# Kernel optimization log

Measured on AMD Instinct MI355X. Metric: run time of the kernel, lower is better.

The kernel has to match this reference:

```python
import jax, jax.numpy as jnp
import numpy as np

B, S, DIN, DQ, DK = 4, 2048, 1024, 64, 64
NEG_INF = -jnp.inf


def _make_mask(sq, sk):
    # Mirrors createMask: causal mask (-inf where key_idx > query_idx),
    # except 3 randomly chosen (row, col) 'global token' pairs left at 0.
    # torch version uses random.sample; we use a fixed numpy RNG for determinism.
    rng = np.random.default_rng(0)
    g_rows = rng.choice(sk, 3, replace=False)  # sampled from range(lrlen)
    g_cols = rng.choice(sq, 3, replace=False)  # sampled from range(sequence_len)
    row = jnp.arange(sq)[:, None]
    col = jnp.arange(sk)[None, :]
    mask = jnp.where(col > row, NEG_INF, 0.0).astype(jnp.float32)
    mask = mask.at[jnp.asarray(g_rows), jnp.asarray(g_cols)].set(0.0)
    return mask  # [sq, sk]


def setup_inputs() -> dict:
    key = jax.random.key(0)
    ks = jax.random.split(key, 9)
    sc = 1.0 / np.sqrt(DIN)
    return {
        "q": jax.random.normal(ks[0], (B, S, DIN), jnp.float32),
        "k": jax.random.normal(ks[1], (B, S, DIN), jnp.float32),
        "v": jax.random.normal(ks[2], (B, S, DIN), jnp.float32),
        "Wq": jax.random.normal(ks[3], (DIN, DQ), jnp.float32) * sc,
        "bq": jax.random.normal(ks[4], (DQ,), jnp.float32) * sc,
        "Wk": jax.random.normal(ks[5], (DIN, DK), jnp.float32) * sc,
        "bk": jax.random.normal(ks[6], (DK,), jnp.float32) * sc,
        "Wv": jax.random.normal(ks[7], (DIN, DK), jnp.float32) * sc,
        "bv": jax.random.normal(ks[8], (DK,), jnp.float32) * sc,
    }


def reference(q, k, v, Wq, bq, Wk, bk, Wv, bv):
    Q = q @ Wq + bq            # [B,S,DQ]
    K = k @ Wk + bk            # [B,S,DK]
    V = v @ Wv + bv            # [B,S,DK]
    scores = jnp.einsum("bqd,bkd->bqk", Q, K)  # [B,S,S]
    mask = _make_mask(scores.shape[-2], scores.shape[-1])
    denom = jnp.asarray(K.shape[-1], jnp.float32) ** 0.5
    # NOTE: original adds mask BEFORE dividing by sqrt(d_k); -inf survives division.
    attn = jax.nn.softmax((scores + mask) / denom, axis=-1)
    return jnp.einsum("bqk,bkd->bqd", attn, V)  # [B,S,DK]
```

## Files before the change

kernel.cpp:

```cpp
#include <hip/hip_runtime.h>
#include <cstdint>
#include <cstddef>
#include <math.h>

#define SEQ    2048
#define NBATCH 4
#define DIN    1024
#define DH     64

typedef __attribute__((ext_vector_type(8))) short  short8;
typedef __attribute__((ext_vector_type(4))) float  floatx4;
typedef __attribute__((ext_vector_type(4))) unsigned short ushort4v;

#define MFMA16(a, b, c) __builtin_amdgcn_mfma_f32_16x16x32_bf16((a), (b), (c), 0, 0, 0)

__device__ __forceinline__ unsigned short f2bf(float x) {
  unsigned u = __float_as_uint(x);
  return (unsigned short)((u + 0x8000u) >> 16);
}
__device__ __forceinline__ float bf2f(unsigned short h) {
  return __uint_as_float(((unsigned)h) << 16);
}

namespace nprng {

struct PCG64 {
  __uint128_t state, inc;
  bool has_uint32;
  uint32_t uinteger;
};

static inline void pcg_step(PCG64 &g) {
  const __uint128_t MULT =
      (((__uint128_t)0x2360ed051fc65da4ULL) << 64) | 0x4385df649fccf645ULL;
  g.state = g.state * MULT + g.inc;
}

static inline uint64_t pcg_output(const PCG64 &g) {
  uint64_t hi = (uint64_t)(g.state >> 64);
  uint64_t lo = (uint64_t)g.state;
  uint64_t x = hi ^ lo;
  unsigned rot = (unsigned)(g.state >> 122) & 63u;
  return (x >> rot) | (x << ((64u - rot) & 63u));
}

static inline uint64_t pcg_next64(PCG64 &g) { pcg_step(g); return pcg_output(g); }

static inline uint32_t pcg_next32(PCG64 &g) {
  if (g.has_uint32) { g.has_uint32 = false; return g.uinteger; }
  uint64_t n = pcg_next64(g);
  g.has_uint32 = true;
  g.uinteger = (uint32_t)(n >> 32);
  return (uint32_t)(n & 0xffffffffu);
}

static inline void pcg_seed_from_seedseq0(PCG64 &g) {
  const uint32_t MULT_A = 0x931e8875u;
  const uint32_t MULT_B = 0x58f38dedu;
  const uint32_t MIX_L  = 0xca01f9ddu;
  const uint32_t MIX_R  = 0x4973f715u;
  uint32_t hc = 0x43b0d7e5u;
  uint32_t pool[4];
  for (int i = 0; i < 4; i++) {
    uint32_t v = 0u;
    v ^= hc; hc *= MULT_A; v *= hc; v ^= v >> 16;
    pool[i] = v;
  }
  for (int is = 0; is < 4; is++) {
    for (int id = 0; id < 4; id++) {
      if (is == id) continue;
      uint32_t h = pool[is];
      h ^= hc; hc *= MULT_A; h *= hc; h ^= h >> 16;
      uint32_t r = (pool[id] * MIX_L) ^ (h * MIX_R);
      r ^= r >> 16;
      pool[id] = r;
    }
  }
  uint32_t hb = 0x8b51f9ddu;
  uint32_t w[8];
  for (int i = 0; i < 8; i++) {
    uint32_t v = pool[i & 3];
    v ^= hb; hb *= MULT_B; v *= hb; v ^= v >> 16;
    w[i] = v;
  }
  uint64_t sv[4];
  for (int k = 0; k < 4; k++)
    sv[k] = (uint64_t)w[2 * k] | ((uint64_t)w[2 * k + 1] << 32);
  __uint128_t initstate = (((__uint128_t)sv[0]) << 64) | sv[1];
  __uint128_t initseq   = (((__uint128_t)sv[2]) << 64) | sv[3];
  g.state = 0; g.inc = (initseq << 1) | 1;
  pcg_step(g);
  g.state += initstate;
  pcg_step(g);
  g.has_uint32 = false; g.uinteger = 0;
}

static inline uint32_t bounded32(PCG64 &g, uint32_t rng ) {
  if (rng == 0) return 0;
  const uint32_t rng_excl = rng + 1u;
  uint64_t m = (uint64_t)pcg_next32(g) * (uint64_t)rng_excl;
  uint32_t leftover = (uint32_t)m;
  if (leftover < rng_excl) {
    const uint32_t threshold = (uint32_t)(0xffffffffu - rng) % rng_excl;
    while (leftover < threshold) {
      m = (uint64_t)pcg_next32(g) * (uint64_t)rng_excl;
      leftover = (uint32_t)m;
    }
  }
  return (uint32_t)(m >> 32);
}

static inline void choice3_2048(PCG64 &g, long long idx[3]) {
  const int pop = 2048, sz = 3;
  uint64_t hs[4] = { (uint64_t)-1, (uint64_t)-1, (uint64_t)-1, (uint64_t)-1 };
  const uint64_t mask = 3;
  for (int j = pop - sz; j < pop; j++) {
    uint64_t val = (uint64_t)bounded32(g, (uint32_t)j);
    uint64_t loc = val & mask;
    while (hs[loc] != (uint64_t)-1 && hs[loc] != val) loc = (loc + 1) & mask;
    if (hs[loc] == (uint64_t)-1) {
      hs[loc] = val;
      idx[j - pop + sz] = (long long)val;
    } else {
      loc = (uint64_t)j & mask;
      while (hs[loc] != (uint64_t)-1) loc = (loc + 1) & mask;
      hs[loc] = (uint64_t)j;
      idx[j - pop + sz] = (long long)j;
    }
  }
  for (int i = 2; i >= 1; i--) {
    uint32_t j = bounded32(g, (uint32_t)i);
    long long t = idx[j]; idx[j] = idx[i]; idx[i] = t;
  }
}

}

__global__ __launch_bounds__(256) void wtrans_kernel(
    const float* __restrict__ Wq, const float* __restrict__ Wk,
    const float* __restrict__ Wv, unsigned short* __restrict__ WT) {
  int idx = blockIdx.x * 256 + threadIdx.x;
  int p   = idx >> 16;
  int rem = idx & 65535;
  int n   = rem >> 10;
  int k   = rem & 1023;
  const float* W = (p == 0) ? Wq : (p == 1) ? Wk : Wv;
  WT[idx] = f2bf(W[k * 64 + n]);
}

__global__ __launch_bounds__(256, 4) void proj_kernel(
    const float* __restrict__ xq, const float* __restrict__ xk,
    const float* __restrict__ xv, const unsigned short* __restrict__ WT,
    const float* __restrict__ bq, const float* __restrict__ bk,
    const float* __restrict__ bv,
    unsigned short* __restrict__ QP, unsigned short* __restrict__ KP,
    unsigned short* __restrict__ VPT) {
  const int proj = blockIdx.y;
  const float* X    = (proj == 0) ? xq : (proj == 1) ? xk : xv;
  const float* bias = (proj == 0) ? bq : (proj == 1) ? bk : bv;

  const int m0   = blockIdx.x * 16;
  const int tid  = threadIdx.x;
  const int w    = tid >> 6;
  const int l    = tid & 63;
  const int quad = l >> 4;
  const int lx   = l & 15;
  const int kb   = w << 8;

  const float* Xr = X + (size_t)(m0 + lx) * DIN + kb + quad * 8;
  const unsigned short* Wb = WT + (size_t)proj * 65536 + kb + quad * 8;
  const unsigned short* Wr0 = Wb + (size_t)(lx)      * 1024;
  const unsigned short* Wr1 = Wb + (size_t)(16 + lx) * 1024;
  const unsigned short* Wr2 = Wb + (size_t)(32 + lx) * 1024;
  const unsigned short* Wr3 = Wb + (size_t)(48 + lx) * 1024;

  floatx4 acc0 = {0.f, 0.f, 0.f, 0.f}, acc1 = acc0, acc2 = acc0, acc3 = acc0;

  float4 xc0 = *(const float4*)(Xr);
  float4 xc1 = *(const float4*)(Xr + 4);
  short8 wc0 = *(const short8*)(Wr0);
  short8 wc1 = *(const short8*)(Wr1);
  short8 wc2 = *(const short8*)(Wr2);
  short8 wc3 = *(const short8*)(Wr3);

  for (int k = 32; k < 256; k += 32) {
    float4 xn0 = *(const float4*)(Xr + k);
    float4 xn1 = *(const float4*)(Xr + k + 4);
    short8 wn0 = *(const short8*)(Wr0 + k);
    short8 wn1 = *(const short8*)(Wr1 + k);
    short8 wn2 = *(const short8*)(Wr2 + k);
    short8 wn3 = *(const short8*)(Wr3 + k);
    short8 af;
    af[0] = f2bf(xc0.x); af[1] = f2bf(xc0.y); af[2] = f2bf(xc0.z); af[3] = f2bf(xc0.w);
    af[4] = f2bf(xc1.x); af[5] = f2bf(xc1.y); af[6] = f2bf(xc1.z); af[7] = f2bf(xc1.w);
    acc0 = MFMA16(af, wc0, acc0);
    acc1 = MFMA16(af, wc1, acc1);
    acc2 = MFMA16(af, wc2, acc2);
    acc3 = MFMA16(af, wc3, acc3);
    xc0 = xn0; xc1 = xn1; wc0 = wn0; wc1 = wn1; wc2 = wn2; wc3 = wn3;
  }
  {
    short8 af;
    af[0] = f2bf(xc0.x); af[1] = f2bf(xc0.y); af[2] = f2bf(xc0.z); af[3] = f2bf(xc0.w);
    af[4] = f2bf(xc1.x); af[5] = f2bf(xc1.y); af[6] = f2bf(xc1.z); af[7] = f2bf(xc1.w);
    acc0 = MFMA16(af, wc0, acc0);
    acc1 = MFMA16(af, wc1, acc1);
    acc2 = MFMA16(af, wc2, acc2);
    acc3 = MFMA16(af, wc3, acc3);
  }

  __shared__ float Cs[4][16][68];
#pragma unroll
  for (int i = 0; i < 4; i++) {
    const int r = quad * 4 + i;
    Cs[w][r][lx]      = acc0[i];
    Cs[w][r][16 + lx] = acc1[i];
    Cs[w][r][32 + lx] = acc2[i];
    Cs[w][r][48 + lx] = acc3[i];
  }
  __syncthreads();

  if (proj < 2) {
    unsigned short* outp = (proj == 0) ? QP : KP;
    const int row = tid >> 4;
    const int d0  = (tid & 15) * 4;
    ushort4v v;
#pragma unroll
    for (int j = 0; j < 4; j++) {
      float s = Cs[0][row][d0 + j] + Cs[1][row][d0 + j] +
                Cs[2][row][d0 + j] + Cs[3][row][d0 + j] + bias[d0 + j];
      v[j] = f2bf(s);
    }
    *(ushort4v*)(outp + (size_t)(m0 + row) * 64 + d0) = v;
  } else {
    const int dim = tid >> 2;
    const int s0  = (tid & 3) * 4;
    const int bq_ = m0 >> 11;
    const int sq  = (m0 & 2047) + s0;
    const float bb = bias[dim];
    ushort4v v;
#pragma unroll
    for (int j = 0; j < 4; j++) {
      float s = Cs[0][s0 + j][dim] + Cs[1][s0 + j][dim] +
                Cs[2][s0 + j][dim] + Cs[3][s0 + j][dim] + bb;
      v[j] = f2bf(s);
    }
    *(ushort4v*)(VPT + ((size_t)bq_ * 64 + dim) * SEQ + sq) = v;
  }
}

__global__ __launch_bounds__(256, 2) void attn_kernel(
    const unsigned short* __restrict__ QP, const unsigned short* __restrict__ KP,
    const unsigned short* __restrict__ VPT, float* __restrict__ out,
    int R0, int C0, int R1, int C1, int R2, int C2) {
  const int b    = blockIdx.y;
  const int bx   = blockIdx.x;
  const int qi   = (bx & 1) ? (127 - (bx >> 1)) : (bx >> 1);
  const int q0   = qi * 16;
  const int tid  = threadIdx.x;
  const int w    = tid >> 6;
  const int l    = tid & 63;
  const int quad = l >> 4;
  const int lx   = l & 15;

  __shared__ unsigned short Ps[4][16][72];
  __shared__ float Os[4][16][64];
  __shared__ float mS[4][16], lS[4][16];
  __shared__ float lgS[3];
  __shared__ int   lgF[3];

  const unsigned short* Qb = QP + ((size_t)b * SEQ + q0) * 64;
  const unsigned short* Kb = KP + (size_t)b * SEQ * 64;
  const unsigned short* Vb = VPT + (size_t)b * 64 * SEQ;

  const short8 aq0 = *(const short8*)(Qb + (size_t)lx * 64 + quad * 8);
  const short8 aq1 = *(const short8*)(Qb + (size_t)lx * 64 + 32 + quad * 8);

  floatx4 O[4];
  float m_i[4], l_i[4];
#pragma unroll
  for (int c = 0; c < 4; c++) O[c] = (floatx4){0.f, 0.f, 0.f, 0.f};
#pragma unroll
  for (int i = 0; i < 4; i++) { m_i[i] = -INFINITY; l_i[i] = 0.f; }

  const int T = (q0 + 79) >> 6;

  for (int t = w; t < T; t += 4) {
    const int k0 = t << 6;
    const bool mT = (t == T - 1);

    short8 kf[8], vf[8];
#pragma unroll
    for (int c = 0; c < 4; c++) {
#pragma unroll
      for (int s = 0; s < 2; s++) {
        kf[c * 2 + s] = *(const short8*)(Kb + (size_t)(k0 + 16 * c + lx) * 64 + s * 32 + quad * 8);
        vf[s * 4 + c] = *(const short8*)(Vb + (size_t)(16 * c + lx) * SEQ + k0 + s * 32 + quad * 8);
      }
    }

    floatx4 sc[4];
#pragma unroll
    for (int c = 0; c < 4; c++) {
      sc[c] = (floatx4){0.f, 0.f, 0.f, 0.f};
      sc[c] = MFMA16(aq0, kf[2 * c], sc[c]);
      sc[c] = MFMA16(aq1, kf[2 * c + 1], sc[c]);
    }

    float mt[4], al[4];
#pragma unroll
    for (int i = 0; i < 4; i++) {
      const int rowg = q0 + quad * 4 + i;
      float vmax = -INFINITY;
#pragma unroll
      for (int c = 0; c < 4; c++) {
        float v = sc[c][i] * 0.125f;
        if (mT && (k0 + 16 * c + lx) > rowg) v = -INFINITY;
        sc[c][i] = v;
        vmax = fmaxf(vmax, v);
      }
      mt[i] = vmax;
    }
#pragma unroll
    for (int i = 0; i < 4; i++) {
#pragma unroll
      for (int off = 8; off >= 1; off >>= 1)
        mt[i] = fmaxf(mt[i], __shfl_xor(mt[i], off));
      const float mn = fmaxf(m_i[i], mt[i]);
      al[i] = __expf(m_i[i] - mn);
      m_i[i] = mn;
      float s = 0.f;
#pragma unroll
      for (int c = 0; c < 4; c++) {
        float p = __expf(sc[c][i] - mn);
        Ps[w][quad * 4 + i][16 * c + lx] = f2bf(p);
        s += p;
      }
#pragma unroll
      for (int off = 8; off >= 1; off >>= 1) s += __shfl_xor(s, off);
      l_i[i] = l_i[i] * al[i] + s;
    }
#pragma unroll
    for (int c = 0; c < 4; c++)
#pragma unroll
      for (int i = 0; i < 4; i++) O[c][i] *= al[i];
    asm volatile("" ::: "memory");
    const short8 pf0 = *(const short8*)&Ps[w][lx][quad * 8];
    const short8 pf1 = *(const short8*)&Ps[w][lx][32 + quad * 8];
#pragma unroll
    for (int c = 0; c < 4; c++) {
      O[c] = MFMA16(pf0, vf[c],     O[c]);
      O[c] = MFMA16(pf1, vf[4 + c], O[c]);
    }
  }

  if (lx == 0) {
#pragma unroll
    for (int i = 0; i < 4; i++) {
      mS[w][quad * 4 + i] = m_i[i];
      lS[w][quad * 4 + i] = l_i[i];
    }
  }
#pragma unroll
  for (int c = 0; c < 4; c++)
#pragma unroll
    for (int i = 0; i < 4; i++) Os[w][quad * 4 + i][16 * c + lx] = O[c][i];

  if (w == 0) {
#pragma unroll
    for (int p = 0; p < 3; p++) {
      const int R = (p == 0) ? R0 : (p == 1) ? R1 : R2;
      const int C = (p == 0) ? C0 : (p == 1) ? C1 : C2;
      const int act = (R >= q0 && R < q0 + 16 && C > R);
      float d = 0.f;
      if (act) {
        const float qv = bf2f(QP[((size_t)b * SEQ + R) * 64 + l]);
        const float kv = bf2f(KP[((size_t)b * SEQ + C) * 64 + l]);
        d = qv * kv;
#pragma unroll
        for (int off = 32; off >= 1; off >>= 1) d += __shfl_xor(d, off);
        d *= 0.125f;
      }
      if (l == 0) { lgF[p] = act; lgS[p] = d; }
    }
  }
  __syncthreads();

  {
    const int row = tid >> 4;
    const int d0  = (tid & 15) * 4;
    const int Rs[3] = {R0, R1, R2};
    const int Cs3[3] = {C0, C1, C2};

    float mf = -INFINITY;
#pragma unroll
    for (int w4 = 0; w4 < 4; w4++) mf = fmaxf(mf, mS[w4][row]);
#pragma unroll
    for (int p = 0; p < 3; p++)
      if (lgF[p] && (Rs[p] - q0) == row) mf = fmaxf(mf, lgS[p]);

    float lf = 0.f;
    float o0 = 0.f, o1 = 0.f, o2 = 0.f, o3 = 0.f;
#pragma unroll
    for (int w4 = 0; w4 < 4; w4++) {
      const float a = __expf(mS[w4][row] - mf);
      lf += a * lS[w4][row];
      const float* op = &Os[w4][row][d0];
      o0 += a * op[0]; o1 += a * op[1]; o2 += a * op[2]; o3 += a * op[3];
    }
#pragma unroll
    for (int p = 0; p < 3; p++) {
      if (lgF[p] && (Rs[p] - q0) == row) {
        const float pe = __expf(lgS[p] - mf);
        lf += pe;
        const int C = Cs3[p];
        o0 += pe * bf2f(Vb[(size_t)(d0 + 0) * SEQ + C]);
        o1 += pe * bf2f(Vb[(size_t)(d0 + 1) * SEQ + C]);
        o2 += pe * bf2f(Vb[(size_t)(d0 + 2) * SEQ + C]);
        o3 += pe * bf2f(Vb[(size_t)(d0 + 3) * SEQ + C]);
      }
    }
    const float inv = 1.0f / lf;
    float4 r;
    r.x = o0 * inv; r.y = o1 * inv; r.z = o2 * inv; r.w = o3 * inv;
    *(float4*)(out + ((size_t)b * SEQ + q0 + row) * 64 + d0) = r;
  }
}

extern "C" void kernel_launch(void* const* d_in, const int* in_sizes, int n_in,
                              void* d_out, int out_size, void* d_ws,
                              size_t ws_size, hipStream_t stream) {
  const float* xq = (const float*)d_in[0];
  const float* xk = (const float*)d_in[1];
  const float* xv = (const float*)d_in[2];
  const float* Wq = (const float*)d_in[3];
  const float* bq = (const float*)d_in[4];
  const float* Wk = (const float*)d_in[5];
  const float* bk = (const float*)d_in[6];
  const float* Wv = (const float*)d_in[7];
  const float* bv = (const float*)d_in[8];
  float* out = (float*)d_out;

  unsigned short* QP  = (unsigned short*)d_ws;
  unsigned short* KP  = QP + (size_t)NBATCH * SEQ * 64;
  unsigned short* VPT = KP + (size_t)NBATCH * SEQ * 64;
  unsigned short* WT  = VPT + (size_t)NBATCH * 64 * SEQ;

  nprng::PCG64 g;
  nprng::pcg_seed_from_seedseq0(g);
  long long rows[3], cols[3];
  nprng::choice3_2048(g, rows);
  nprng::choice3_2048(g, cols);

  wtrans_kernel<<<768, 256, 0, stream>>>(Wq, Wk, Wv, WT);

  dim3 pgrid(512, 3);
  proj_kernel<<<pgrid, 256, 0, stream>>>(xq, xk, xv, WT, bq, bk, bv, QP, KP, VPT);

  dim3 agrid(SEQ / 16, NBATCH);
  attn_kernel<<<agrid, 256, 0, stream>>>(
      QP, KP, VPT, out, (int)rows[0], (int)cols[0], (int)rows[1], (int)cols[1],
      (int)rows[2], (int)cols[2]);
}
```

Before: 188.5 us.

## Restructure projection GEMM to stage X in LDS and split output columns across waves

The projection kernel now processes 32 rows per block instead of 16. X is loaded coalesced, converted to bf16 and staged in shared memory in 256-wide K chunks, with register double-buffering of the next chunk's X and W. Each wave now owns 16 output columns over the full K range instead of a K-slice, so the cross-wave reduction through shared memory goes away. Output stores are widened to 8 elements. The cost is more registers (launch bounds lowered to 3), LDS barriers per chunk, and half as many blocks.

```diff
diff --git a/kernel.cpp b/kernel.cpp
--- a/kernel.cpp
+++ b/kernel.cpp
@@ -148,7 +148,7 @@
   WT[idx] = f2bf(W[k * 64 + n]);
 }
 
-__global__ __launch_bounds__(256, 4) void proj_kernel(
+__global__ __launch_bounds__(256, 3) void proj_kernel(
     const float* __restrict__ xq, const float* __restrict__ xk,
     const float* __restrict__ xv, const unsigned short* __restrict__ WT,
     const float* __restrict__ bq, const float* __restrict__ bk,
@@ -159,93 +159,91 @@
   const float* X    = (proj == 0) ? xq : (proj == 1) ? xk : xv;
   const float* bias = (proj == 0) ? bq : (proj == 1) ? bk : bv;
 
-  const int m0   = blockIdx.x * 16;
+  const int m0   = blockIdx.x * 32;
   const int tid  = threadIdx.x;
   const int w    = tid >> 6;
   const int l    = tid & 63;
   const int quad = l >> 4;
   const int lx   = l & 15;
-  const int kb   = w << 8;
-
-  const float* Xr = X + (size_t)(m0 + lx) * DIN + kb + quad * 8;
-  const unsigned short* Wb = WT + (size_t)proj * 65536 + kb + quad * 8;
-  const unsigned short* Wr0 = Wb + (size_t)(lx)      * 1024;
-  const unsigned short* Wr1 = Wb + (size_t)(16 + lx) * 1024;
-  const unsigned short* Wr2 = Wb + (size_t)(32 + lx) * 1024;
-  const unsigned short* Wr3 = Wb + (size_t)(48 + lx) * 1024;
-
-  floatx4 acc0 = {0.f, 0.f, 0.f, 0.f}, acc1 = acc0, acc2 = acc0, acc3 = acc0;
-
-  float4 xc0 = *(const float4*)(Xr);
-  float4 xc1 = *(const float4*)(Xr + 4);
-  short8 wc0 = *(const short8*)(Wr0);
-  short8 wc1 = *(const short8*)(Wr1);
-  short8 wc2 = *(const short8*)(Wr2);
-  short8 wc3 = *(const short8*)(Wr3);
-
-  for (int k = 32; k < 256; k += 32) {
-    float4 xn0 = *(const float4*)(Xr + k);
-    float4 xn1 = *(const float4*)(Xr + k + 4);
-    short8 wn0 = *(const short8*)(Wr0 + k);
-    short8 wn1 = *(const short8*)(Wr1 + k);
-    short8 wn2 = *(const short8*)(Wr2 + k);
-    short8 wn3 = *(const short8*)(Wr3 + k);
-    short8 af;
-    af[0] = f2bf(xc0.x); af[1] = f2bf(xc0.y); af[2] = f2bf(xc0.z); af[3] = f2bf(xc0.w);
-    af[4] = f2bf(xc1.x); af[5] = f2bf(xc1.y); af[6] = f2bf(xc1.z); af[7] = f2bf(xc1.w);
-    acc0 = MFMA16(af, wc0, acc0);
-    acc1 = MFMA16(af, wc1, acc1);
-    acc2 = MFMA16(af, wc2, acc2);
-    acc3 = MFMA16(af, wc3, acc3);
-    xc0 = xn0; xc1 = xn1; wc0 = wn0; wc1 = wn1; wc2 = wn2; wc3 = wn3;
-  }
-  {
-    short8 af;
-    af[0] = f2bf(xc0.x); af[1] = f2bf(xc0.y); af[2] = f2bf(xc0.z); af[3] = f2bf(xc0.w);
-    af[4] = f2bf(xc1.x); af[5] = f2bf(xc1.y); af[6] = f2bf(xc1.z); af[7] = f2bf(xc1.w);
-    acc0 = MFMA16(af, wc0, acc0);
-    acc1 = MFMA16(af, wc1, acc1);
-    acc2 = MFMA16(af, wc2, acc2);
-    acc3 = MFMA16(af, wc3, acc3);
-  }
-
-  __shared__ float Cs[4][16][68];
+
+  __shared__ unsigned short Xs[32][264];
+  __shared__ float Cs[32][68];
+
+  const float* Xg = X + (size_t)m0 * DIN;
+  const unsigned short* Wrow = WT + (size_t)proj * 65536 + (size_t)(w * 16 + lx) * 1024 + quad * 8;
+
+  float4 xg[8];
+  short8 wc[8], wn[8];
+
+#pragma unroll
+  for (int i = 0; i < 8; i++)
+    xg[i] = *(const float4*)(Xg + (size_t)(4 * i + w) * DIN + l * 4);
+#pragma unroll
+  for (int ks = 0; ks < 8; ks++)
+    wc[ks] = *(const short8*)(Wrow + ks * 32);
+
+  floatx4 acc0 = {0.f, 0.f, 0.f, 0.f}, acc1 = acc0;
+
+#pragma unroll
+  for (int c = 0; c < 4; c++) {
+#pragma unroll
+    for (int i = 0; i < 8; i++) {
+      ushort4v v;
+      v[0] = f2bf(xg[i].x); v[1] = f2bf(xg[i].y);
+      v[2] = f2bf(xg[i].z); v[3] = f2bf(xg[i].w);
+      *(ushort4v*)&Xs[4 * i + w][l * 4] = v;
+    }
+    if (c < 3) {
+      const int k0n = (c + 1) * 256;
+#pragma unroll
+      for (int i = 0; i < 8; i++)
+        xg[i] = *(const float4*)(Xg + (size_t)(4 * i + w) * DIN + k0n + l * 4);
+#pragma unroll
+      for (int ks = 0; ks < 8; ks++)
+        wn[ks] = *(const short8*)(Wrow + k0n + ks * 32);
+    }
+    __syncthreads();
+
+#pragma unroll
+    for (int ks = 0; ks < 8; ks++) {
+      const short8 a0 = *(const short8*)&Xs[lx][ks * 32 + quad * 8];
+      const short8 a1 = *(const short8*)&Xs[16 + lx][ks * 32 + quad * 8];
+      acc0 = MFMA16(a0, wc[ks], acc0);
+      acc1 = MFMA16(a1, wc[ks], acc1);
+    }
+    __syncthreads();
+
+    if (c < 3) {
+#pragma unroll
+      for (int ks = 0; ks < 8; ks++) wc[ks] = wn[ks];
+    }
+  }
+
+  const float bb = bias[w * 16 + lx];
 #pragma unroll
   for (int i = 0; i < 4; i++) {
-    const int r = quad * 4 + i;
-    Cs[w][r][lx]      = acc0[i];
-    Cs[w][r][16 + lx] = acc1[i];
-    Cs[w][r][32 + lx] = acc2[i];
-    Cs[w][r][48 + lx] = acc3[i];
+    Cs[quad * 4 + i][w * 16 + lx]      = acc0[i] + bb;
+    Cs[16 + quad * 4 + i][w * 16 + lx] = acc1[i] + bb;
   }
   __syncthreads();
 
   if (proj < 2) {
     unsigned short* outp = (proj == 0) ? QP : KP;
-    const int row = tid >> 4;
-    const int d0  = (tid & 15) * 4;
-    ushort4v v;
-#pragma unroll
-    for (int j = 0; j < 4; j++) {
-      float s = Cs[0][row][d0 + j] + Cs[1][row][d0 + j] +
-                Cs[2][row][d0 + j] + Cs[3][row][d0 + j] + bias[d0 + j];
-      v[j] = f2bf(s);
-    }
-    *(ushort4v*)(outp + (size_t)(m0 + row) * 64 + d0) = v;
+    const int row = tid >> 3;
+    const int d0  = (tid & 7) * 8;
+    short8 v;
+#pragma unroll
+    for (int j = 0; j < 8; j++) v[j] = (short)f2bf(Cs[row][d0 + j]);
+    *(short8*)(outp + (size_t)(m0 + row) * 64 + d0) = v;
   } else {
     const int dim = tid >> 2;
-    const int s0  = (tid & 3) * 4;
+    const int s0  = (tid & 3) * 8;
     const int bq_ = m0 >> 11;
     const int sq  = (m0 & 2047) + s0;
-    const float bb = bias[dim];
-    ushort4v v;
-#pragma unroll
-    for (int j = 0; j < 4; j++) {
-      float s = Cs[0][s0 + j][dim] + Cs[1][s0 + j][dim] +
-                Cs[2][s0 + j][dim] + Cs[3][s0 + j][dim] + bb;
-      v[j] = f2bf(s);
-    }
-    *(ushort4v*)(VPT + ((size_t)bq_ * 64 + dim) * SEQ + sq) = v;
+    short8 v;
+#pragma unroll
+    for (int j = 0; j < 8; j++) v[j] = (short)f2bf(Cs[s0 + j][dim]);
+    *(short8*)(VPT + ((size_t)bq_ * 64 + dim) * SEQ + sq) = v;
   }
 }
 
@@ -454,7 +452,7 @@
 
   wtrans_kernel<<<768, 256, 0, stream>>>(Wq, Wk, Wv, WT);
 
-  dim3 pgrid(512, 3);
+  dim3 pgrid(256, 3);
   proj_kernel<<<pgrid, 256, 0, stream>>>(xq, xk, xv, WT, bq, bk, bv, QP, KP, VPT);
 
   dim3 agrid(SEQ / 16, NBATCH);
```

After: 175.6 us. 6.8% less time.
